# Optimization experiments

Hardware: AMD Instinct MI355X
Metric: run time of the kernel (lower is better)

## Reference

```python
import jax, jax.numpy as jnp
import numpy as np


def setup_inputs() -> dict:
    key = jax.random.key(0)
    ks = jax.random.split(key, 6)
    B, S, D, L = 4, 4096, 1024, 8192
    return {
        "inputs": jax.random.normal(ks[0], (B, S, D), dtype=jnp.float32),
        "W_w": jax.random.normal(ks[1], (D, D), dtype=jnp.float32) * (1.0 / np.sqrt(D)),
        "W_b": jax.random.normal(ks[2], (D,), dtype=jnp.float32) * 0.02,
        "U_w": jax.random.normal(ks[3], (L, D), dtype=jnp.float32) * (1.0 / np.sqrt(D)),
        "final_w": jax.random.normal(ks[4], (L, D), dtype=jnp.float32) * (1.0 / np.sqrt(D)),
        "final_b": jax.random.normal(ks[5], (L,), dtype=jnp.float32) * 0.02,
    }


def reference(inputs, W_w, W_b, U_w, final_w, final_b):
    # Z = tanh(W(inputs)): [B,S,D]
    Z = jnp.tanh(jnp.einsum("bsd,ed->bse", inputs, W_w) + W_b)
    # scores = U.weight @ Z^T: [B,L,S], softmax over seq
    scores = jnp.einsum("ld,bsd->bls", U_w, Z)
    alpha = jax.nn.softmax(scores, axis=2)
    # hidden = alpha @ inputs: [B,L,D]
    hidden = jnp.einsum("bls,bsd->bld", alpha, inputs)
    # logits = sum_d final_w[l,d]*hidden[b,l,d] + final_b[l]: [B,L]
    logits = jnp.einsum("ld,bld->bl", final_w, hidden) + final_b
    return logits
```

## Files before the change

### kernel.cpp

```cpp
#include <hip/hip_runtime.h>

typedef __attribute__((ext_vector_type(8))) short bf16x8;
typedef __attribute__((ext_vector_type(4))) float f32x4;
typedef unsigned short us;

#define DEVINL __device__ __forceinline__
#define AS1 __attribute__((address_space(1)))
#define AS3 __attribute__((address_space(3)))

constexpr int BB = 4, SS = 4096, DD = 1024, LL = 8192;
constexpr int LT_ = 128;
constexpr int STB = 256;
constexpr int BK  = 32;
constexpr int NST = SS / STB;
constexpr int KST = DD / BK;
constexpr int NU  = NST * KST;
constexpr int U_SH = LT_ * BK;
constexpr int Z_SH = STB * BK;
constexpr int SLOT_SH = 2*U_SH + 2*Z_SH;
constexpr int ZKST = DD / 64;

DEVINL unsigned short f2bf(float f){
  union { float f; unsigned u; } a; a.f = f;
  unsigned r = a.u + 0x7fffu + ((a.u >> 16) & 1u);
  return (unsigned short)(r >> 16);
}

DEVINL void gll16(const void* src, void* dst){
  __builtin_amdgcn_global_load_lds((const AS1 unsigned int*)src,
                                   (AS3 unsigned int*)dst, 16, 0, 0);
}

__global__ void conv_kernel(const float4* __restrict__ in,
                            ushort4* __restrict__ out, int n4){
  int stride = gridDim.x * blockDim.x;
  for (int i = blockIdx.x*blockDim.x + threadIdx.x; i < n4; i += stride){
    float4 v = in[i];
    ushort4 o;
    o.x = f2bf(v.x); o.y = f2bf(v.y); o.z = f2bf(v.z); o.w = f2bf(v.w);
    out[i] = o;
  }
}

constexpr int ZTILE = 128 * 64;

DEVINL bf16x8 zread_frag(const us* tile, int row, int chunk){
  return *(const AS3 bf16x8*)(tile + row*64 + ((chunk ^ (row & 7)) << 3));
}

DEVINL void stage_tile128(const us* __restrict__ g0, int row0, int d0,
                          us* ldsbase, int wave, int lane){
#pragma unroll
  for (int it = 0; it < 4; ++it){
    int off  = it*4096 + wave*1024 + lane*16;
    int row  = off >> 7;
    int slot = (off >> 4) & 7;
    int scol = (slot ^ (row & 7)) << 3;
    gll16(g0 + (size_t)(row0 + row) * DD + d0 + scol,
          ldsbase + ((it*4096 + wave*1024) >> 1));
  }
}

__global__ __launch_bounds__(256, 2) void zgemm_kernel(
    const us* __restrict__ X, const us* __restrict__ W,
    const float* __restrict__ Wb, us* __restrict__ Z)
{
  __shared__ __align__(16) us lds[2*ZTILE];
  const int bid = blockIdx.x;
  const int tm = bid & 127;
  const int tn = bid >> 7;
  const int tid = threadIdx.x, wave = tid >> 6, lane = tid & 63;
  const int wl = wave >> 1, wn = wave & 1;
  const int g = lane >> 4, cc = lane & 15;

  f32x4 acc[4][4] = {};
#pragma unroll 1
  for (int ks = 0; ks < ZKST; ++ks){
    __syncthreads();
    stage_tile128(X, tm*128, ks*64, lds,         wave, lane);
    stage_tile128(W, tn*128, ks*64, lds + ZTILE, wave, lane);
    __syncthreads();
#pragma unroll
    for (int ksub = 0; ksub < 2; ++ksub){
      bf16x8 af[4], bfr[4];
#pragma unroll
      for (int f = 0; f < 4; ++f) af[f]  = zread_frag(lds,         wl*64 + f*16 + cc, ksub*4 + g);
#pragma unroll
      for (int f = 0; f < 4; ++f) bfr[f] = zread_frag(lds + ZTILE, wn*64 + f*16 + cc, ksub*4 + g);
#pragma unroll
      for (int fm = 0; fm < 4; ++fm)
#pragma unroll
        for (int fn = 0; fn < 4; ++fn)
          acc[fm][fn] = __builtin_amdgcn_mfma_f32_16x16x32_bf16(af[fm], bfr[fn], acc[fm][fn], 0, 0, 0);
    }
  }
#pragma unroll
  for (int fm = 0; fm < 4; ++fm)
#pragma unroll
    for (int fn = 0; fn < 4; ++fn)
#pragma unroll
      for (int r = 0; r < 4; ++r){
        int row = tm*128 + wl*64 + fm*16 + 4*g + r;
        int col = tn*128 + wn*64 + fn*16 + cc;
        float y = acc[fm][fn][r] + Wb[col];
        float e2 = __expf(2.f * y);
        float t = 1.f - 2.f / (e2 + 1.f);
        Z[(size_t)row*DD + col] = f2bf(t);
      }
}

__global__ __launch_bounds__(512, 2) void fused_kernel(
    const us* __restrict__ U, const us* __restrict__ F,
    const us* __restrict__ Z, const us* __restrict__ X,
    float* __restrict__ pse, float* __restrict__ pac)
{
  __shared__ __align__(16) us lds[3 * SLOT_SH];

  const int h = blockIdx.x;
  const int xcd = h & 7, j = h >> 3;
  const int lt = xcd * 8 + (j & 7);
  const int b  = j >> 3;

  const int tid = threadIdx.x;
  const int wave = tid >> 6, lane = tid & 63;
  const int wl = wave >> 2, ws = wave & 3;
  const int g = lane >> 4, cc = lane & 15;

  const us* Ub = U + (size_t)lt * LT_ * DD;
  const us* Fb = F + (size_t)lt * LT_ * DD;
  const us* Zb = Z + (size_t)b * SS * DD;
  const us* Xb = X + (size_t)b * SS * DD;

  const int lg   = ((tid & 3) - (tid >> 3)) & 3;
  const int offA = (tid >> 2) * DD + lg * 8;

  const int sl8 = ((g + (cc >> 1)) & 3) * 8;

  const int arow = (wl*64 + cc) * BK + sl8;
  const int brow = (ws*64 + cc) * BK + sl8;

  f32x4 sacc[4][4] = {}, gacc[4][4] = {};
  float se_pk = 0.f, ac_pk = 0.f;

  auto stage_unit = [&](int n){
    int nn = (n >= NU) ? n - NU : n;
    us* sb = lds + (n % 3) * SLOT_SH;
    const int k32 = (nn & 31) * BK;
    const size_t stoff = (size_t)(nn >> 5) * STB * DD;
    gll16(Ub + k32 + offA, sb + tid*8);
    gll16(Fb + k32 + offA, sb + U_SH + tid*8);
    const us* pZ = Zb + stoff + k32 + offA;
    gll16(pZ,          sb + 2*U_SH + tid*8);
    gll16(pZ + 128*DD, sb + 2*U_SH + 4096 + tid*8);
    const us* pX = Xb + stoff + k32 + offA;
    gll16(pX,          sb + 2*U_SH + Z_SH + tid*8);
    gll16(pX + 128*DD, sb + 2*U_SH + Z_SH + 4096 + tid*8);
  };

  stage_unit(0);
  stage_unit(1);
  stage_unit(2);
  asm volatile("s_waitcnt vmcnt(12)" ::: "memory");
  __builtin_amdgcn_s_barrier();

  bf16x8 pa[4], pb[4];
#pragma unroll
  for (int f = 0; f < 4; ++f)
    pa[f] = *(const AS3 bf16x8*)(lds + arow + f*16*BK);
#pragma unroll
  for (int f = 0; f < 4; ++f)
    pb[f] = *(const AS3 bf16x8*)(lds + 2*U_SH + brow + f*16*BK);

#pragma unroll 1
  for (int u = 0; u < NU; ++u){
    const us* sb = lds + (u % 3) * SLOT_SH;
    const us* tF = sb + U_SH;
    const us* tX = sb + 2*U_SH + Z_SH;

    bf16x8 a1[4], b1[4];
#pragma unroll
    for (int f = 0; f < 4; ++f)
      a1[f] = *(const AS3 bf16x8*)(tF + arow + f*16*BK);
#pragma unroll
    for (int f = 0; f < 4; ++f)
      b1[f] = *(const AS3 bf16x8*)(tX + brow + f*16*BK);
    __builtin_amdgcn_sched_barrier(0);

    __builtin_amdgcn_s_setprio(1);
#pragma unroll
    for (int fm = 0; fm < 4; ++fm)
#pragma unroll
      for (int fn = 0; fn < 4; ++fn)
        sacc[fm][fn] = __builtin_amdgcn_mfma_f32_16x16x32_bf16(pa[fm], pb[fn], sacc[fm][fn], 0, 0, 0);
    __builtin_amdgcn_s_setprio(0);

    __builtin_amdgcn_s_setprio(1);
#pragma unroll
    for (int fm = 0; fm < 4; ++fm)
#pragma unroll
      for (int fn = 0; fn < 4; ++fn)
        gacc[fm][fn] = __builtin_amdgcn_mfma_f32_16x16x32_bf16(a1[fm], b1[fn], gacc[fm][fn], 0, 0, 0);
    __builtin_amdgcn_s_setprio(0);

    asm volatile("s_waitcnt vmcnt(6)" ::: "memory");
    __builtin_amdgcn_s_barrier();
    stage_unit(u + 3);

    {
      int un = u + 1; if (un >= NU) un -= NU;
      const us* sn = lds + (un % 3) * SLOT_SH;
#pragma unroll
      for (int f = 0; f < 4; ++f)
        pa[f] = *(const AS3 bf16x8*)(sn + arow + f*16*BK);
#pragma unroll
      for (int f = 0; f < 4; ++f)
        pb[f] = *(const AS3 bf16x8*)(sn + 2*U_SH + brow + f*16*BK);
    }
    __builtin_amdgcn_sched_barrier(0);

    if ((u & 31) == 31){
#pragma unroll
      for (int fm = 0; fm < 4; ++fm)
#pragma unroll
        for (int r = 0; r < 4; ++r){
          float ps = 0.f, pg = 0.f;
#pragma unroll
          for (int fn = 0; fn < 4; ++fn){
            float p = __expf(sacc[fm][fn][r]);
            ps += p;
            pg += p * gacc[fm][fn][r];
          }
#pragma unroll
          for (int m = 1; m < 16; m <<= 1){
            ps += __shfl_xor(ps, m, 64);
            pg += __shfl_xor(pg, m, 64);
          }
          bool sel = (cc == fm*4 + r);
          se_pk += sel ? ps : 0.f;
          ac_pk += sel ? pg : 0.f;
        }
#pragma unroll
      for (int fm = 0; fm < 4; ++fm)
#pragma unroll
        for (int fn = 0; fn < 4; ++fn){
          sacc[fm][fn] = f32x4{0.f, 0.f, 0.f, 0.f};
          gacc[fm][fn] = f32x4{0.f, 0.f, 0.f, 0.f};
        }
    }
  }

  {
    int row = (cc >> 2)*16 + 4*g + (cc & 3);
    int l = lt*LT_ + wl*64 + row;
    size_t idx = ((size_t)b*LL + l)*4 + ws;
    pse[idx] = se_pk;
    pac[idx] = ac_pk;
  }
}

__global__ void combine_kernel(const float* __restrict__ pse, const float* __restrict__ pac,
                               const float* __restrict__ fb, float* __restrict__ out)
{
  int i = blockIdx.x*blockDim.x + threadIdx.x;
  if (i >= BB*LL) return;
  int l = i & (LL - 1);
  float s = 0.f, a = 0.f;
#pragma unroll
  for (int k = 0; k < 4; ++k){
    s += pse[(size_t)i*4 + k];
    a += pac[(size_t)i*4 + k];
  }
  out[i] = a / s + fb[l];
}

extern "C" void kernel_launch(void* const* d_in, const int* in_sizes, int n_in,
                              void* d_out, int out_size, void* d_ws, size_t ws_size,
                              hipStream_t stream)
{
  const float* inp = (const float*)d_in[0];
  const float* Ww  = (const float*)d_in[1];
  const float* Wb  = (const float*)d_in[2];
  const float* Uw  = (const float*)d_in[3];
  const float* Fw  = (const float*)d_in[4];
  const float* fb  = (const float*)d_in[5];
  float* out = (float*)d_out;

  char* ws = (char*)d_ws;
  us* Xbf = (us*)(ws);
  us* Zbf = (us*)(ws + (size_t)32*1024*1024);
  us* Ubf = (us*)(ws + (size_t)64*1024*1024);
  us* Fbf = (us*)(ws + (size_t)80*1024*1024);
  us* Wbf = (us*)(ws + (size_t)96*1024*1024);
  float* pse = (float*)(ws + (size_t)98*1024*1024);
  float* pac = (float*)(ws + (size_t)99*1024*1024);

  conv_kernel<<<2048, 256, 0, stream>>>((const float4*)inp, (ushort4*)Xbf, BB*SS*DD/4);
  conv_kernel<<<256,  256, 0, stream>>>((const float4*)Ww,  (ushort4*)Wbf, DD*DD/4);
  conv_kernel<<<1024, 256, 0, stream>>>((const float4*)Uw,  (ushort4*)Ubf, LL*DD/4);
  conv_kernel<<<1024, 256, 0, stream>>>((const float4*)Fw,  (ushort4*)Fbf, LL*DD/4);

  zgemm_kernel<<<128*8, 256, 0, stream>>>(Xbf, Wbf, Wb, Zbf);
  fused_kernel<<<256, 512, 0, stream>>>(Ubf, Fbf, Zbf, Xbf, pse, pac);
  combine_kernel<<<(BB*LL + 255)/256, 256, 0, stream>>>(pse, pac, fb, out);
}
```

Measured before the change: 632.3 us.

## Load U/F operand fragments directly from global into registers, stage only Z/X in LDS

The A-side operands (U and final_w tiles) are no longer staged through LDS; each wave loads its bf16x8 fragments straight from global memory into double-buffered registers one unit ahead. LDS slots now hold only the Z and X tiles, halving LDS footprint and LDS read traffic. The loop is unrolled by two with ping-pong register buffers, and the barrier and next-stage issue are placed between the two MFMA groups. This relies on L2/L1 hits for the repeatedly reread U/F rows and adds register pressure and uncoalesced-ish global loads in the hot loop.

```diff
diff --git a/kernel.cpp b/kernel.cpp
--- a/kernel.cpp
+++ b/kernel.cpp
@@ -15,9 +15,8 @@
 constexpr int NST = SS / STB;
 constexpr int KST = DD / BK;
 constexpr int NU  = NST * KST;
-constexpr int U_SH = LT_ * BK;
 constexpr int Z_SH = STB * BK;
-constexpr int SLOT_SH = 2*U_SH + 2*Z_SH;
+constexpr int SLOT_SH = 2 * Z_SH;
 constexpr int ZKST = DD / 64;
 
 DEVINL unsigned short f2bf(float f){
@@ -132,12 +131,15 @@
   const us* Xb = X + (size_t)b * SS * DD;
 
   const int lg   = ((tid & 3) - (tid >> 3)) & 3;
-  const int offA = (tid >> 2) * DD + lg * 8;
+  const int offB = (tid >> 2) * DD + lg * 8;
 
   const int sl8 = ((g + (cc >> 1)) & 3) * 8;
-
-  const int arow = (wl*64 + cc) * BK + sl8;
   const int brow = (ws*64 + cc) * BK + sl8;
+
+  int aoffA[4];
+#pragma unroll
+  for (int f = 0; f < 4; ++f)
+    aoffA[f] = (wl*64 + f*16 + cc) * DD + g*8;
 
   f32x4 sacc[4][4] = {}, gacc[4][4] = {};
   float se_pk = 0.f, ac_pk = 0.f;
@@ -147,106 +149,102 @@
     us* sb = lds + (n % 3) * SLOT_SH;
     const int k32 = (nn & 31) * BK;
     const size_t stoff = (size_t)(nn >> 5) * STB * DD;
-    gll16(Ub + k32 + offA, sb + tid*8);
-    gll16(Fb + k32 + offA, sb + U_SH + tid*8);
-    const us* pZ = Zb + stoff + k32 + offA;
-    gll16(pZ,          sb + 2*U_SH + tid*8);
-    gll16(pZ + 128*DD, sb + 2*U_SH + 4096 + tid*8);
-    const us* pX = Xb + stoff + k32 + offA;
-    gll16(pX,          sb + 2*U_SH + Z_SH + tid*8);
-    gll16(pX + 128*DD, sb + 2*U_SH + Z_SH + 4096 + tid*8);
+    const us* pZ = Zb + stoff + k32 + offB;
+    gll16(pZ,          sb + tid*8);
+    gll16(pZ + 128*DD, sb + 4096 + tid*8);
+    const us* pX = Xb + stoff + k32 + offB;
+    gll16(pX,          sb + Z_SH + tid*8);
+    gll16(pX + Z_SH/2*0 + 128*DD, sb + Z_SH + 4096 + tid*8);
+  };
+
+  auto epilogue = [&](){
+#pragma unroll
+    for (int fm = 0; fm < 4; ++fm)
+#pragma unroll
+      for (int r = 0; r < 4; ++r){
+        float ps = 0.f, pg = 0.f;
+#pragma unroll
+        for (int fn = 0; fn < 4; ++fn){
+          float p = __expf(sacc[fm][fn][r]);
+          ps += p;
+          pg += p * gacc[fm][fn][r];
+        }
+#pragma unroll
+        for (int m = 1; m < 16; m <<= 1){
+          ps += __shfl_xor(ps, m, 64);
+          pg += __shfl_xor(pg, m, 64);
+        }
+        bool sel = (cc == fm*4 + r);
+        se_pk += sel ? ps : 0.f;
+        ac_pk += sel ? pg : 0.f;
+      }
+#pragma unroll
+    for (int fm = 0; fm < 4; ++fm)
+#pragma unroll
+      for (int fn = 0; fn < 4; ++fn){
+        sacc[fm][fn] = f32x4{0.f, 0.f, 0.f, 0.f};
+        gacc[fm][fn] = f32x4{0.f, 0.f, 0.f, 0.f};
+      }
+  };
+
+  auto body = [&](int u, bf16x8 (&uaC)[4], bf16x8 (&faC)[4],
+                         bf16x8 (&uaN)[4], bf16x8 (&faN)[4]){
+    const us* sb = lds + (u % 3) * SLOT_SH;
+    bf16x8 z0[4], x1[4];
+#pragma unroll
+    for (int f = 0; f < 4; ++f)
+      z0[f] = *(const AS3 bf16x8*)(sb + brow + f*16*BK);
+#pragma unroll
+    for (int f = 0; f < 4; ++f)
+      x1[f] = *(const AS3 bf16x8*)(sb + Z_SH + brow + f*16*BK);
+
+    int un = u + 1; if (un >= NU) un -= NU;
+    const int kn = (un & 31) * BK;
+#pragma unroll
+    for (int f = 0; f < 4; ++f) uaN[f] = *(const bf16x8*)(Ub + kn + aoffA[f]);
+#pragma unroll
+    for (int f = 0; f < 4; ++f) faN[f] = *(const bf16x8*)(Fb + kn + aoffA[f]);
+
+    __builtin_amdgcn_s_setprio(1);
+#pragma unroll
+    for (int fm = 0; fm < 4; ++fm)
+#pragma unroll
+      for (int fn = 0; fn < 4; ++fn)
+        sacc[fm][fn] = __builtin_amdgcn_mfma_f32_16x16x32_bf16(uaC[fm], z0[fn], sacc[fm][fn], 0, 0, 0);
+    __builtin_amdgcn_s_setprio(0);
+
+    asm volatile("s_waitcnt lgkmcnt(0)" ::: "memory");
+    __builtin_amdgcn_sched_barrier(0);
+    asm volatile("s_waitcnt vmcnt(12)" ::: "memory");
+    __builtin_amdgcn_s_barrier();
+    stage_unit(u + 3);
+
+    __builtin_amdgcn_s_setprio(1);
+#pragma unroll
+    for (int fm = 0; fm < 4; ++fm)
+#pragma unroll
+      for (int fn = 0; fn < 4; ++fn)
+        gacc[fm][fn] = __builtin_amdgcn_mfma_f32_16x16x32_bf16(faC[fm], x1[fn], gacc[fm][fn], 0, 0, 0);
+    __builtin_amdgcn_s_setprio(0);
+
+    if ((u & 31) == 31) epilogue();
   };
 
   stage_unit(0);
   stage_unit(1);
   stage_unit(2);
-  asm volatile("s_waitcnt vmcnt(12)" ::: "memory");
+  bf16x8 uaA[4], faA[4], uaB[4], faB[4];
+#pragma unroll
+  for (int f = 0; f < 4; ++f) uaA[f] = *(const bf16x8*)(Ub + aoffA[f]);
+#pragma unroll
+  for (int f = 0; f < 4; ++f) faA[f] = *(const bf16x8*)(Fb + aoffA[f]);
+  asm volatile("s_waitcnt vmcnt(16)" ::: "memory");
   __builtin_amdgcn_s_barrier();
 
-  bf16x8 pa[4], pb[4];
-#pragma unroll
-  for (int f = 0; f < 4; ++f)
-    pa[f] = *(const AS3 bf16x8*)(lds + arow + f*16*BK);
-#pragma unroll
-  for (int f = 0; f < 4; ++f)
-    pb[f] = *(const AS3 bf16x8*)(lds + 2*U_SH + brow + f*16*BK);
-
 #pragma unroll 1
-  for (int u = 0; u < NU; ++u){
-    const us* sb = lds + (u % 3) * SLOT_SH;
-    const us* tF = sb + U_SH;
-    const us* tX = sb + 2*U_SH + Z_SH;
-
-    bf16x8 a1[4], b1[4];
-#pragma unroll
-    for (int f = 0; f < 4; ++f)
-      a1[f] = *(const AS3 bf16x8*)(tF + arow + f*16*BK);
-#pragma unroll
-    for (int f = 0; f < 4; ++f)
-      b1[f] = *(const AS3 bf16x8*)(tX + brow + f*16*BK);
-    __builtin_amdgcn_sched_barrier(0);
-
-    __builtin_amdgcn_s_setprio(1);
-#pragma unroll
-    for (int fm = 0; fm < 4; ++fm)
-#pragma unroll
-      for (int fn = 0; fn < 4; ++fn)
-        sacc[fm][fn] = __builtin_amdgcn_mfma_f32_16x16x32_bf16(pa[fm], pb[fn], sacc[fm][fn], 0, 0, 0);
-    __builtin_amdgcn_s_setprio(0);
-
-    __builtin_amdgcn_s_setprio(1);
-#pragma unroll
-    for (int fm = 0; fm < 4; ++fm)
-#pragma unroll
-      for (int fn = 0; fn < 4; ++fn)
-        gacc[fm][fn] = __builtin_amdgcn_mfma_f32_16x16x32_bf16(a1[fm], b1[fn], gacc[fm][fn], 0, 0, 0);
-    __builtin_amdgcn_s_setprio(0);
-
-    asm volatile("s_waitcnt vmcnt(6)" ::: "memory");
-    __builtin_amdgcn_s_barrier();
-    stage_unit(u + 3);
-
-    {
-      int un = u + 1; if (un >= NU) un -= NU;
-      const us* sn = lds + (un % 3) * SLOT_SH;
-#pragma unroll
-      for (int f = 0; f < 4; ++f)
-        pa[f] = *(const AS3 bf16x8*)(sn + arow + f*16*BK);
-#pragma unroll
-      for (int f = 0; f < 4; ++f)
-        pb[f] = *(const AS3 bf16x8*)(sn + 2*U_SH + brow + f*16*BK);
-    }
-    __builtin_amdgcn_sched_barrier(0);
-
-    if ((u & 31) == 31){
-#pragma unroll
-      for (int fm = 0; fm < 4; ++fm)
-#pragma unroll
-        for (int r = 0; r < 4; ++r){
-          float ps = 0.f, pg = 0.f;
-#pragma unroll
-          for (int fn = 0; fn < 4; ++fn){
-            float p = __expf(sacc[fm][fn][r]);
-            ps += p;
-            pg += p * gacc[fm][fn][r];
-          }
-#pragma unroll
-          for (int m = 1; m < 16; m <<= 1){
-            ps += __shfl_xor(ps, m, 64);
-            pg += __shfl_xor(pg, m, 64);
-          }
-          bool sel = (cc == fm*4 + r);
-          se_pk += sel ? ps : 0.f;
-          ac_pk += sel ? pg : 0.f;
-        }
-#pragma unroll
-      for (int fm = 0; fm < 4; ++fm)
-#pragma unroll
-        for (int fn = 0; fn < 4; ++fn){
-          sacc[fm][fn] = f32x4{0.f, 0.f, 0.f, 0.f};
-          gacc[fm][fn] = f32x4{0.f, 0.f, 0.f, 0.f};
-        }
-    }
+  for (int u = 0; u < NU; u += 2){
+    body(u,     uaA, faA, uaB, faB);
+    body(u + 1, uaB, faB, uaA, faA);
   }
 
   {
```

Result: slower. 1.308 ms (median of 3 runs) (+106.8%).
